# Optimization experiments

Hardware: AMD Instinct MI355X
Metric: run time of the kernel (lower is better)

The kernel has to match this reference:

```python
import math
import jax, jax.numpy as jnp
import numpy as np

B, S, D, L = 8, 2048, 1024, 2


def setup_inputs() -> dict:
    key = jax.random.key(0)
    ks = jax.random.split(key, 16)
    sc = 1.0 / math.sqrt(D)
    mask = jax.random.randint(ks[0], (B, S, S), 0, 2).astype(bool)
    reps = jax.random.normal(ks[1], (B, S, D), dtype=jnp.float32)
    def w(k, shape):
        return jax.random.uniform(k, shape, jnp.float32, -sc, sc)
    return {
        "batch_tk_mask": mask,
        "batch_tk_reps": reps,
        "W_ih": w(ks[2], (L, D, D)), "W_hh": w(ks[3], (L, D, D)),
        "b_ih": w(ks[4], (L, D)), "b_hh": w(ks[5], (L, D)),
        "Wq": w(ks[6], (L, D, D)), "bq": w(ks[7], (L, D)),
        "Wk": w(ks[8], (L, D, D)), "bk": w(ks[9], (L, D)),
        "Wv": w(ks[10], (L, D, D)), "bv": w(ks[11], (L, D)),
        "Wo": w(ks[12], (L, D, D)), "bo": w(ks[13], (L, D)),
    }


def _rnn(x, Wih, Whh, bih, bhh):
    # x: (B,S,D) -> hidden states (B,S,D); h_t = tanh(x_t Wih^T + b_ih + h_{t-1} Whh^T + b_hh)
    h0 = jnp.zeros((x.shape[0], Whh.shape[0]), x.dtype)
    xs = jnp.swapaxes(x, 0, 1)  # (S,B,D)

    def step(h, xt):
        h = jnp.tanh(xt @ Wih.T + bih + h @ Whh.T + bhh)
        return h, h

    _, hs = jax.lax.scan(step, h0, xs)
    return jnp.swapaxes(hs, 0, 1)  # (B,S,D)


def reference(batch_tk_mask, batch_tk_reps, W_ih, W_hh, b_ih, b_hh, Wq, bq, Wk, bk, Wv, bv, Wo, bo):
    scale = 1.0 / math.sqrt(batch_tk_reps.shape[-1])  # sqrt(d_hid)
    batch = batch_tk_reps
    for l in range(L):
        h = _rnn(batch, W_ih[l], W_hh[l], b_ih[l], b_hh[l])  # (B,S,D)
        q = h @ Wq[l].T + bq[l]
        k = h @ Wk[l].T + bk[l]
        v = h @ Wv[l].T + bv[l]
        attn = jnp.einsum("bsd,btd->bst", q, k) * scale  # (B,S,S)
        attn = jnp.where(batch_tk_mask, jnp.float32(-1e9), attn)
        attn = jax.nn.softmax(attn, axis=-1)
        batch = jnp.einsum("bst,btd->bsd", attn, v) @ Wo[l].T + bo[l]
        # dropout p=0.0 -> identity
    return batch
```

## Files before the change

kernel.cpp:

```cpp
#include <hip/hip_runtime.h>
#include <hip/hip_bf16.h>

#define BATCH 8
#define SEQ   2048
#define DIM   1024
#define NLAYER 2

typedef float  f32x4 __attribute__((ext_vector_type(4)));
typedef short  s16x8 __attribute__((ext_vector_type(8)));
typedef unsigned short u16x4 __attribute__((ext_vector_type(4)));

__device__ __forceinline__ void split_bf16(float x, unsigned short& hi, unsigned short& lo) {
  const __hip_bfloat16 hb = __float2bfloat16(x);
  hi = *reinterpret_cast<const unsigned short*>(&hb);
  const float hf = __bfloat162float(hb);
  lo = (unsigned short)(__float_as_uint(x - hf) >> 16);
}

__global__ __launch_bounds__(256)
void split_mat(const float* __restrict__ W, unsigned short* __restrict__ Wh,
               unsigned short* __restrict__ Wl)
{
  const int i = (blockIdx.x * 256 + threadIdx.x) * 4;
  const float4 v = *(const float4*)&W[i];
  unsigned short h0,h1,h2,h3,l0,l1,l2,l3;
  split_bf16(v.x, h0, l0); split_bf16(v.y, h1, l1);
  split_bf16(v.z, h2, l2); split_bf16(v.w, h3, l3);
  *(u16x4*)&Wh[i] = (u16x4){h0, h1, h2, h3};
  *(u16x4*)&Wl[i] = (u16x4){l0, l1, l2, l3};
}

template<int TRANSB>
__global__ __launch_bounds__(256)
void gemm_bf16x3(const float* __restrict__ A, const float* __restrict__ B,
                 const float* __restrict__ bias, float* __restrict__ C,
                 int M, int N, int K, float alpha,
                 long long strideA, long long strideB, long long strideC)
{
  constexpr int LK = 40;
  __shared__ unsigned short Ah[128 * LK], Al[128 * LK];
  __shared__ unsigned short Bh[128 * LK], Bl[128 * LK];

  const int z = blockIdx.z;
  A += (size_t)z * strideA;
  B += (size_t)z * strideB;
  C += (size_t)z * strideC;

  const int tid  = threadIdx.x;
  const int row0 = blockIdx.x * 128;
  const int col0 = blockIdx.y * 128;
  const int w    = tid >> 6;
  const int lane = tid & 63;
  const int m0   = (w >> 1) * 64;
  const int n0   = (w & 1) * 64;
  const int half = lane >> 4;
  const int mr   = lane & 15;

  f32x4 acc[4][4];
#pragma unroll
  for (int i = 0; i < 4; ++i)
#pragma unroll
    for (int j = 0; j < 4; ++j) acc[i][j] = (f32x4){0.f, 0.f, 0.f, 0.f};

  for (int k0 = 0; k0 < K; k0 += 32) {
    __syncthreads();
    {
      const int r = tid >> 3, c4 = tid & 7;
#pragma unroll
      for (int rep = 0; rep < 4; ++rep) {
        const int row = r + rep * 32;
        const float4 v = *(const float4*)&A[(size_t)(row0 + row) * K + k0 + c4 * 4];
        unsigned short h0,h1,h2,h3,l0,l1,l2,l3;
        split_bf16(v.x, h0, l0); split_bf16(v.y, h1, l1);
        split_bf16(v.z, h2, l2); split_bf16(v.w, h3, l3);
        *(u16x4*)&Ah[row * LK + c4 * 4] = (u16x4){h0, h1, h2, h3};
        *(u16x4*)&Al[row * LK + c4 * 4] = (u16x4){l0, l1, l2, l3};
      }
    }
    if (TRANSB) {
      const int r = tid >> 3, c4 = tid & 7;
#pragma unroll
      for (int rep = 0; rep < 4; ++rep) {
        const int row = r + rep * 32;
        const float4 v = *(const float4*)&B[(size_t)(col0 + row) * K + k0 + c4 * 4];
        unsigned short h0,h1,h2,h3,l0,l1,l2,l3;
        split_bf16(v.x, h0, l0); split_bf16(v.y, h1, l1);
        split_bf16(v.z, h2, l2); split_bf16(v.w, h3, l3);
        *(u16x4*)&Bh[row * LK + c4 * 4] = (u16x4){h0, h1, h2, h3};
        *(u16x4*)&Bl[row * LK + c4 * 4] = (u16x4){l0, l1, l2, l3};
      }
    } else {
      const int kk8 = tid >> 5, n4 = tid & 31;
#pragma unroll
      for (int rep = 0; rep < 4; ++rep) {
        const int kk = kk8 + rep * 8;
        const float4 v = *(const float4*)&B[(size_t)(k0 + kk) * N + col0 + n4 * 4];
        unsigned short h, l;
        split_bf16(v.x, h, l); Bh[(n4*4+0)*LK + kk] = h; Bl[(n4*4+0)*LK + kk] = l;
        split_bf16(v.y, h, l); Bh[(n4*4+1)*LK + kk] = h; Bl[(n4*4+1)*LK + kk] = l;
        split_bf16(v.z, h, l); Bh[(n4*4+2)*LK + kk] = h; Bl[(n4*4+2)*LK + kk] = l;
        split_bf16(v.w, h, l); Bh[(n4*4+3)*LK + kk] = h; Bl[(n4*4+3)*LK + kk] = l;
      }
    }
    __syncthreads();

    s16x8 ah[4], al[4], bh[4], bl[4];
#pragma unroll
    for (int i = 0; i < 4; ++i) {
      ah[i] = *(const s16x8*)&Ah[(m0 + i*16 + mr) * LK + half * 8];
      al[i] = *(const s16x8*)&Al[(m0 + i*16 + mr) * LK + half * 8];
      bh[i] = *(const s16x8*)&Bh[(n0 + i*16 + mr) * LK + half * 8];
      bl[i] = *(const s16x8*)&Bl[(n0 + i*16 + mr) * LK + half * 8];
    }
#pragma unroll
    for (int i = 0; i < 4; ++i)
#pragma unroll
      for (int j = 0; j < 4; ++j) {
        acc[i][j] = __builtin_amdgcn_mfma_f32_16x16x32_bf16(ah[i], bh[j], acc[i][j], 0, 0, 0);
        acc[i][j] = __builtin_amdgcn_mfma_f32_16x16x32_bf16(ah[i], bl[j], acc[i][j], 0, 0, 0);
        acc[i][j] = __builtin_amdgcn_mfma_f32_16x16x32_bf16(al[i], bh[j], acc[i][j], 0, 0, 0);
      }
  }

#pragma unroll
  for (int j = 0; j < 4; ++j) {
    const int col = col0 + n0 + j * 16 + mr;
    const float bb = bias ? bias[col] : 0.f;
#pragma unroll
    for (int i = 0; i < 4; ++i) {
#pragma unroll
      for (int q = 0; q < 4; ++q) {
        const int row = row0 + m0 + i * 16 + half * 4 + q;
        C[(size_t)row * N + col] = fmaf(alpha, acc[i][j][q], bb);
      }
    }
  }
}

__global__ __launch_bounds__(256)
void gemm_bsplit(const float* __restrict__ A,
                 const unsigned short* __restrict__ Bhg,
                 const unsigned short* __restrict__ Blg,
                 const float* __restrict__ bias, float* __restrict__ C,
                 int M, int N, int K, float alpha)
{
  constexpr int LK = 40;
  __shared__ unsigned short Ah[128 * LK], Al[128 * LK];
  __shared__ unsigned short Bh[128 * LK], Bl[128 * LK];

  const int tid  = threadIdx.x;
  const int row0 = blockIdx.x * 128;
  const int col0 = blockIdx.y * 128;
  const int w    = tid >> 6;
  const int lane = tid & 63;
  const int m0   = (w >> 1) * 64;
  const int n0   = (w & 1) * 64;
  const int half = lane >> 4;
  const int mr   = lane & 15;

  f32x4 acc[4][4];
#pragma unroll
  for (int i = 0; i < 4; ++i)
#pragma unroll
    for (int j = 0; j < 4; ++j) acc[i][j] = (f32x4){0.f, 0.f, 0.f, 0.f};

  for (int k0 = 0; k0 < K; k0 += 32) {
    __syncthreads();
    {
      const int r = tid >> 3, c4 = tid & 7;
#pragma unroll
      for (int rep = 0; rep < 4; ++rep) {
        const int row = r + rep * 32;
        const float4 v = *(const float4*)&A[(size_t)(row0 + row) * K + k0 + c4 * 4];
        unsigned short h0,h1,h2,h3,l0,l1,l2,l3;
        split_bf16(v.x, h0, l0); split_bf16(v.y, h1, l1);
        split_bf16(v.z, h2, l2); split_bf16(v.w, h3, l3);
        *(u16x4*)&Ah[row * LK + c4 * 4] = (u16x4){h0, h1, h2, h3};
        *(u16x4*)&Al[row * LK + c4 * 4] = (u16x4){l0, l1, l2, l3};
      }
    }
    {
      const int r = tid >> 3, c4 = tid & 7;
#pragma unroll
      for (int rep = 0; rep < 4; ++rep) {
        const int row = r + rep * 32;
        const size_t off = (size_t)(col0 + row) * K + k0 + c4 * 4;
        *(u16x4*)&Bh[row * LK + c4 * 4] = *(const u16x4*)&Bhg[off];
        *(u16x4*)&Bl[row * LK + c4 * 4] = *(const u16x4*)&Blg[off];
      }
    }
    __syncthreads();

    s16x8 ah[4], al[4], bh[4], bl[4];
#pragma unroll
    for (int i = 0; i < 4; ++i) {
      ah[i] = *(const s16x8*)&Ah[(m0 + i*16 + mr) * LK + half * 8];
      al[i] = *(const s16x8*)&Al[(m0 + i*16 + mr) * LK + half * 8];
      bh[i] = *(const s16x8*)&Bh[(n0 + i*16 + mr) * LK + half * 8];
      bl[i] = *(const s16x8*)&Bl[(n0 + i*16 + mr) * LK + half * 8];
    }
#pragma unroll
    for (int i = 0; i < 4; ++i)
#pragma unroll
      for (int j = 0; j < 4; ++j) {
        acc[i][j] = __builtin_amdgcn_mfma_f32_16x16x32_bf16(ah[i], bh[j], acc[i][j], 0, 0, 0);
        acc[i][j] = __builtin_amdgcn_mfma_f32_16x16x32_bf16(ah[i], bl[j], acc[i][j], 0, 0, 0);
        acc[i][j] = __builtin_amdgcn_mfma_f32_16x16x32_bf16(al[i], bh[j], acc[i][j], 0, 0, 0);
      }
  }

#pragma unroll
  for (int j = 0; j < 4; ++j) {
    const int col = col0 + n0 + j * 16 + mr;
    const float bb = bias ? bias[col] : 0.f;
#pragma unroll
    for (int i = 0; i < 4; ++i) {
#pragma unroll
      for (int q = 0; q < 4; ++q) {
        const int row = row0 + m0 + i * 16 + half * 4 + q;
        C[(size_t)row * N + col] = fmaf(alpha, acc[i][j][q], bb);
      }
    }
  }
}

__device__ __forceinline__ float fast_tanh(float x) {
  const float a = fabsf(x);
  const float e = __expf(2.0f * a);
  const float t = 1.0f - 2.0f / (e + 1.0f);
  return copysignf(t, x);
}

__global__ __launch_bounds__(512, 1)
void rnn_scan(const float* __restrict__ Pre, float* __restrict__ Hout,
              const float* __restrict__ Whh, const float* __restrict__ bhh)
{
  __shared__ float wS[32][DIM];
  __shared__ __align__(16) float hbuf[2][DIM];
  __shared__ float pS[8][8];
  const int b    = blockIdx.x & 7;
  const int p    = blockIdx.x >> 3;
  const int wv   = threadIdx.x >> 6;
  const int lane = threadIdx.x & 63;
  const int fl   = ((lane & 1) << 1) | ((lane >> 1) & 1);

  const float* PreB = Pre  + (size_t)b * SEQ * DIM;
  float*       HB   = Hout + (size_t)b * SEQ * DIM;

  for (int i = threadIdx.x; i < 32 * (DIM / 4); i += 512) {
    const int row = i >> 8, c4 = i & 255;
    *(f32x4*)&wS[row][c4 * 4] =
        *(const f32x4*)&Whh[(size_t)(p * 32 + row) * DIM + c4 * 4];
  }
  __syncthreads();

  const bool w0lane = (wv == 0) && (lane < 32);
  const float biasv = w0lane ? bhh[p * 32 + lane] : 0.f;

  for (int t = 0; t < SEQ; ++t) {
    float pre = 0.f;
    if (w0lane) pre = PreB[(size_t)t * DIM + p * 32 + lane];

    f32x4 wr[4][4];
    if (wv != 0) {
#pragma unroll
      for (int r = 0; r < 4; ++r) {
        wr[r][0] = *(const f32x4*)&wS[wv * 4 + r][  0 + lane * 4];
        wr[r][1] = *(const f32x4*)&wS[wv * 4 + r][256 + lane * 4];
        wr[r][2] = *(const f32x4*)&wS[wv * 4 + r][512 + lane * 4];
        wr[r][3] = *(const f32x4*)&wS[wv * 4 + r][768 + lane * 4];
      }
    }

    if (t > 0) {
      if (wv == 0) {
        const float* hp = HB + (size_t)(t - 1) * DIM;
        const float* q0 = hp +   0 + lane * 4;
        const float* q1 = hp + 256 + lane * 4;
        const float* q2 = hp + 512 + lane * 4;
        const float* q3 = hp + 768 + lane * 4;
        f32x4 m0, m1, m2, m3;
        while (true) {
          f32x4 f0, f1, f2, f3;
          asm volatile(
            "global_load_dwordx4 %0, %4, off sc0\n\t"
            "global_load_dwordx4 %1, %5, off sc0\n\t"
            "global_load_dwordx4 %2, %6, off sc0\n\t"
            "global_load_dwordx4 %3, %7, off sc0\n\t"
            "s_waitcnt vmcnt(0)"
            : "=&v"(f0), "=&v"(f1), "=&v"(f2), "=&v"(f3)
            : "v"(q0), "v"(q1), "v"(q2), "v"(q3));
          bool gf = true;
#pragma unroll
          for (int j = 0; j < 4; ++j) {
            gf = gf && (__float_as_uint(f0[j]) != 0xFFFFFFFFu)
                    && (__float_as_uint(f1[j]) != 0xFFFFFFFFu)
                    && (__float_as_uint(f2[j]) != 0xFFFFFFFFu)
                    && (__float_as_uint(f3[j]) != 0xFFFFFFFFu);
          }
          if (__all(gf)) { m0 = f0; m1 = f1; m2 = f2; m3 = f3; break; }

          f32x4 s0, s1, s2, s3;
          asm volatile(
            "global_load_dwordx4 %0, %4, off sc0 sc1\n\t"
            "global_load_dwordx4 %1, %5, off sc0 sc1\n\t"
            "global_load_dwordx4 %2, %6, off sc0 sc1\n\t"
            "global_load_dwordx4 %3, %7, off sc0 sc1\n\t"
            "s_waitcnt vmcnt(0)"
            : "=&v"(s0), "=&v"(s1), "=&v"(s2), "=&v"(s3)
            : "v"(q0), "v"(q1), "v"(q2), "v"(q3));
          bool gm = true;
#pragma unroll
          for (int j = 0; j < 4; ++j) {
            m0[j] = (__float_as_uint(f0[j]) != 0xFFFFFFFFu) ? f0[j] : s0[j];
            m1[j] = (__float_as_uint(f1[j]) != 0xFFFFFFFFu) ? f1[j] : s1[j];
            m2[j] = (__float_as_uint(f2[j]) != 0xFFFFFFFFu) ? f2[j] : s2[j];
            m3[j] = (__float_as_uint(f3[j]) != 0xFFFFFFFFu) ? f3[j] : s3[j];
            gm = gm && (__float_as_uint(m0[j]) != 0xFFFFFFFFu)
                    && (__float_as_uint(m1[j]) != 0xFFFFFFFFu)
                    && (__float_as_uint(m2[j]) != 0xFFFFFFFFu)
                    && (__float_as_uint(m3[j]) != 0xFFFFFFFFu);
          }
          if (__all(gm)) break;
        }
        *(f32x4*)&hbuf[t & 1][  0 + lane * 4] = m0;
        *(f32x4*)&hbuf[t & 1][256 + lane * 4] = m1;
        *(f32x4*)&hbuf[t & 1][512 + lane * 4] = m2;
        *(f32x4*)&hbuf[t & 1][768 + lane * 4] = m3;
#pragma unroll
        for (int r = 0; r < 4; ++r) {
          wr[r][0] = *(const f32x4*)&wS[wv * 4 + r][  0 + lane * 4];
          wr[r][1] = *(const f32x4*)&wS[wv * 4 + r][256 + lane * 4];
          wr[r][2] = *(const f32x4*)&wS[wv * 4 + r][512 + lane * 4];
          wr[r][3] = *(const f32x4*)&wS[wv * 4 + r][768 + lane * 4];
        }
      }
      __syncthreads();
      const f32x4 h0 = *(const f32x4*)&hbuf[t & 1][  0 + lane * 4];
      const f32x4 h1 = *(const f32x4*)&hbuf[t & 1][256 + lane * 4];
      const f32x4 h2 = *(const f32x4*)&hbuf[t & 1][512 + lane * 4];
      const f32x4 h3 = *(const f32x4*)&hbuf[t & 1][768 + lane * 4];
      float acc[4];
#pragma unroll
      for (int r = 0; r < 4; ++r) {
        float a = 0.f;
        a = fmaf(wr[r][0].x, h0.x, fmaf(wr[r][0].y, h0.y,
            fmaf(wr[r][0].z, h0.z, fmaf(wr[r][0].w, h0.w, a))));
        a = fmaf(wr[r][1].x, h1.x, fmaf(wr[r][1].y, h1.y,
            fmaf(wr[r][1].z, h1.z, fmaf(wr[r][1].w, h1.w, a))));
        a = fmaf(wr[r][2].x, h2.x, fmaf(wr[r][2].y, h2.y,
            fmaf(wr[r][2].z, h2.z, fmaf(wr[r][2].w, h2.w, a))));
        a = fmaf(wr[r][3].x, h3.x, fmaf(wr[r][3].y, h3.y,
            fmaf(wr[r][3].z, h3.z, fmaf(wr[r][3].w, h3.w, a))));
        acc[r] = a;
      }
#pragma unroll
      for (int m = 0; m < 2; ++m) {
        const int mask = 1 << m;
        const int nv   = 2 >> m;
        const bool up  = (lane & mask) != 0;
#pragma unroll
        for (int r = 0; r < nv; ++r) {
          const float lo = up ? acc[r + nv] : acc[r];
          const float hi = up ? acc[r] : acc[r + nv];
          acc[r] = lo + __shfl_xor(hi, mask);
        }
      }
#pragma unroll
      for (int off = 4; off < 64; off <<= 1) acc[0] += __shfl_xor(acc[0], off);

      if (lane < 4) pS[wv][fl] = acc[0];
      __syncthreads();
    }

    if (w0lane) {
      float s = (t > 0) ? (pre + pS[lane >> 2][lane & 3] + biasv)
                        : (pre + biasv);
      const float v = fast_tanh(s);
      float* dst = HB + (size_t)t * DIM + p * 32 + lane;
      asm volatile(
        "global_store_dword %0, %1, off sc0\n\t"
        "global_store_dword %0, %1, off sc0 sc1"
        :: "v"(dst), "v"(v));
    }
  }
}

__global__ __launch_bounds__(256)
void softmax_mask(float* __restrict__ S, const unsigned char* __restrict__ mask)
{
  const size_t row = (size_t)blockIdx.y * gridDim.x + blockIdx.x;
  float* p = S + row * SEQ;
  const unsigned char* mrow = mask + row * SEQ;
  __shared__ float buf[SEQ];
  __shared__ float red[4];
  const int tid = threadIdx.x, lane = tid & 63, wv = tid >> 6;

  float mx = -1e30f;
  for (int i = tid; i < SEQ; i += 256) {
    const float v = mrow[i] ? -1e9f : p[i];
    buf[i] = v;
    mx = fmaxf(mx, v);
  }
#pragma unroll
  for (int off = 1; off < 64; off <<= 1) mx = fmaxf(mx, __shfl_xor(mx, off));
  if (lane == 0) red[wv] = mx;
  __syncthreads();
  mx = fmaxf(fmaxf(red[0], red[1]), fmaxf(red[2], red[3]));

  float s = 0.f;
  for (int i = tid; i < SEQ; i += 256) {
    const float e = __expf(buf[i] - mx);
    buf[i] = e;
    s += e;
  }
#pragma unroll
  for (int off = 1; off < 64; off <<= 1) s += __shfl_xor(s, off);
  __syncthreads();
  if (lane == 0) red[wv] = s;
  __syncthreads();
  s = red[0] + red[1] + red[2] + red[3];
  const float inv = 1.f / s;
  for (int i = tid; i < SEQ; i += 256) p[i] = buf[i] * inv;
}

extern "C" void kernel_launch(void* const* d_in, const int* in_sizes, int n_in,
                              void* d_out, int out_size, void* d_ws, size_t ws_size,
                              hipStream_t stream)
{
  (void)in_sizes; (void)n_in; (void)out_size;
  const unsigned char* mask = (const unsigned char*)d_in[0];
  const float* reps = (const float*)d_in[1];
  const float* Wih  = (const float*)d_in[2];
  const float* Whh  = (const float*)d_in[3];
  const float* bih  = (const float*)d_in[4];
  const float* bhh  = (const float*)d_in[5];
  const float* Wq   = (const float*)d_in[6];
  const float* bq   = (const float*)d_in[7];
  const float* Wk   = (const float*)d_in[8];
  const float* bk   = (const float*)d_in[9];
  const float* Wv   = (const float*)d_in[10];
  const float* bv   = (const float*)d_in[11];
  const float* Wo   = (const float*)d_in[12];
  const float* bo   = (const float*)d_in[13];
  float* out = (float*)d_out;

  char* ws = (char*)d_ws;
  float* Hb = (float*)(ws);
  float* Qb = (float*)(ws + ((size_t)64  << 20));
  float* Kb = (float*)(ws + ((size_t)128 << 20));
  float* Vb = (float*)(ws + ((size_t)192 << 20));
  float* Sb = (float*)(ws + ((size_t)256 << 20));
  const size_t needFull = ((size_t)256 << 20) + (size_t)BATCH * SEQ * SEQ * 4;
  const bool fullS = ws_size >= needFull;
  const size_t MM = (size_t)DIM * DIM;
  unsigned short* wsp = (unsigned short*)(ws + needFull);
  const bool presplit = fullS && (ws_size >= needFull + ((size_t)20 << 20));
  const size_t hBytes = (size_t)BATCH * SEQ * DIM * 4;

  const int M1 = BATCH * SEQ;
  const float scale = 0.03125f;
  const dim3 blk(256);
  const dim3 projGrid(M1/128, DIM/128, 1);
  const long long sSD = (long long)SEQ * DIM;
  const long long sSS = (long long)SEQ * SEQ;
  const int splitGrid = (int)(MM / (256 * 4));

  const float* X = reps;
  for (int l = 0; l < NLAYER; ++l) {
    const size_t wof = (size_t)l * DIM * DIM;
    const size_t bof = (size_t)l * DIM;
    float* Y = (l == NLAYER - 1) ? out : Qb;

    hipMemsetAsync(Hb, 0xFF, hBytes, stream);
    if (presplit) {
      split_mat<<<splitGrid, blk, 0, stream>>>(Wih + wof, wsp + 0*MM, wsp + 1*MM);
      split_mat<<<splitGrid, blk, 0, stream>>>(Wq  + wof, wsp + 2*MM, wsp + 3*MM);
      split_mat<<<splitGrid, blk, 0, stream>>>(Wk  + wof, wsp + 4*MM, wsp + 5*MM);
      split_mat<<<splitGrid, blk, 0, stream>>>(Wv  + wof, wsp + 6*MM, wsp + 7*MM);
      split_mat<<<splitGrid, blk, 0, stream>>>(Wo  + wof, wsp + 8*MM, wsp + 9*MM);
    }

    if (presplit)
      gemm_bsplit<<<projGrid, blk, 0, stream>>>(
          X, wsp + 0*MM, wsp + 1*MM, bih + bof, Kb, M1, DIM, DIM, 1.f);
    else
      gemm_bf16x3<1><<<projGrid, blk, 0, stream>>>(
          X, Wih + wof, bih + bof, Kb, M1, DIM, DIM, 1.f, 0, 0, 0);

    rnn_scan<<<dim3(256), dim3(512), 0, stream>>>(Kb, Hb, Whh + wof, bhh + bof);

    if (presplit) {
      gemm_bsplit<<<projGrid, blk, 0, stream>>>(
          Hb, wsp + 2*MM, wsp + 3*MM, bq + bof, Qb, M1, DIM, DIM, 1.f);
      gemm_bsplit<<<projGrid, blk, 0, stream>>>(
          Hb, wsp + 4*MM, wsp + 5*MM, bk + bof, Kb, M1, DIM, DIM, 1.f);
      gemm_bsplit<<<projGrid, blk, 0, stream>>>(
          Hb, wsp + 6*MM, wsp + 7*MM, bv + bof, Vb, M1, DIM, DIM, 1.f);
    } else {
      gemm_bf16x3<1><<<projGrid, blk, 0, stream>>>(
          Hb, Wq + wof, bq + bof, Qb, M1, DIM, DIM, 1.f, 0, 0, 0);
      gemm_bf16x3<1><<<projGrid, blk, 0, stream>>>(
          Hb, Wk + wof, bk + bof, Kb, M1, DIM, DIM, 1.f, 0, 0, 0);
      gemm_bf16x3<1><<<projGrid, blk, 0, stream>>>(
          Hb, Wv + wof, bv + bof, Vb, M1, DIM, DIM, 1.f, 0, 0, 0);
    }

    if (fullS) {
      gemm_bf16x3<1><<<dim3(SEQ/128, SEQ/128, BATCH), blk, 0, stream>>>(
          Qb, Kb, nullptr, Sb, SEQ, SEQ, DIM, scale, sSD, sSD, sSS);
      softmax_mask<<<dim3(SEQ, BATCH), blk, 0, stream>>>(Sb, mask);
      gemm_bf16x3<0><<<dim3(SEQ/128, DIM/128, BATCH), blk, 0, stream>>>(
          Sb, Vb, nullptr, Hb, SEQ, DIM, SEQ, 1.f, sSS, sSD, sSD);
    } else {
      for (int bb = 0; bb < BATCH; ++bb) {
        gemm_bf16x3<1><<<dim3(SEQ/128, SEQ/128, 1), blk, 0, stream>>>(
            Qb + (size_t)bb * sSD, Kb + (size_t)bb * sSD, nullptr, Sb,
            SEQ, SEQ, DIM, scale, 0, 0, 0);
        softmax_mask<<<dim3(SEQ, 1), blk, 0, stream>>>(Sb, mask + (size_t)bb * sSS);
        gemm_bf16x3<0><<<dim3(SEQ/128, DIM/128, 1), blk, 0, stream>>>(
            Sb, Vb + (size_t)bb * sSD, nullptr, Hb + (size_t)bb * sSD,
            SEQ, DIM, SEQ, 1.f, 0, 0, 0);
      }
    }

    if (presplit)
      gemm_bsplit<<<projGrid, blk, 0, stream>>>(
          Hb, wsp + 8*MM, wsp + 9*MM, bo + bof, Y, M1, DIM, DIM, 1.f);
    else
      gemm_bf16x3<1><<<projGrid, blk, 0, stream>>>(
          Hb, Wo + wof, bo + bof, Y, M1, DIM, DIM, 1.f, 0, 0, 0);
    X = Y;
  }
}
```

Before: 10.71 ms.

## Emit pre-split bf16 Q/K and transposed V to remove per-tile splitting in attention GEMMs

When the workspace allows pre-splitting, the Q and K projections now write bf16 hi/lo planes directly. V is written in fp32 and then transposed and split by a new vtrans kernel. The QK^T GEMM loads the pre-split A and B operands, and the PV GEMM reads the transposed split V. This removes the repeated fp32-to-bf16x2 conversion, and the strided non-transposed B load, from the large attention GEMMs. The cost is an extra transpose kernel and reuse of buffers as bf16 planes, which depends on the aliasing being correct.

```diff
diff --git a/kernel.cpp b/kernel.cpp
--- a/kernel.cpp
+++ b/kernel.cpp
@@ -30,21 +30,57 @@
   *(u16x4*)&Wl[i] = (u16x4){l0, l1, l2, l3};
 }
 
-template<int TRANSB>
 __global__ __launch_bounds__(256)
-void gemm_bf16x3(const float* __restrict__ A, const float* __restrict__ B,
+void vtrans(const float* __restrict__ V, unsigned short* __restrict__ Th,
+            unsigned short* __restrict__ Tl)
+{
+  __shared__ float t[64][65];
+  const int z = blockIdx.z;
+  V  += (size_t)z * SEQ * DIM;
+  Th += (size_t)z * (size_t)DIM * SEQ;
+  Tl += (size_t)z * (size_t)DIM * SEQ;
+  const int s0 = blockIdx.x * 64, d0 = blockIdx.y * 64;
+  const int tid = threadIdx.x;
+#pragma unroll
+  for (int rep = 0; rep < 4; ++rep) {
+    const int idx = rep * 256 + tid;
+    const int r = idx >> 4, c = idx & 15;
+    const float4 v = *(const float4*)&V[(size_t)(s0 + r) * DIM + d0 + c * 4];
+    t[c*4+0][r] = v.x; t[c*4+1][r] = v.y; t[c*4+2][r] = v.z; t[c*4+3][r] = v.w;
+  }
+  __syncthreads();
+#pragma unroll
+  for (int rep = 0; rep < 4; ++rep) {
+    const int idx = rep * 256 + tid;
+    const int r = idx >> 4, c = idx & 15;
+    unsigned short h[4], l[4];
+#pragma unroll
+    for (int j = 0; j < 4; ++j) split_bf16(t[r][c*4+j], h[j], l[j]);
+    const size_t off = (size_t)(d0 + r) * SEQ + s0 + c * 4;
+    *(u16x4*)&Th[off] = (u16x4){h[0], h[1], h[2], h[3]};
+    *(u16x4*)&Tl[off] = (u16x4){l[0], l[1], l[2], l[3]};
+  }
+}
+
+template<int WS>
+__global__ __launch_bounds__(256)
+void gemm_bsplit(const float* __restrict__ A,
+                 const unsigned short* __restrict__ Bhg,
+                 const unsigned short* __restrict__ Blg,
                  const float* __restrict__ bias, float* __restrict__ C,
+                 unsigned short* __restrict__ Ch, unsigned short* __restrict__ Cl,
                  int M, int N, int K, float alpha,
-                 long long strideA, long long strideB, long long strideC)
+                 long long sA, long long sB, long long sC)
 {
   constexpr int LK = 40;
   __shared__ unsigned short Ah[128 * LK], Al[128 * LK];
   __shared__ unsigned short Bh[128 * LK], Bl[128 * LK];
 
   const int z = blockIdx.z;
-  A += (size_t)z * strideA;
-  B += (size_t)z * strideB;
-  C += (size_t)z * strideC;
+  A += (size_t)z * sA;
+  Bhg += (size_t)z * sB;  Blg += (size_t)z * sB;
+  if (WS) { Ch += (size_t)z * sC; Cl += (size_t)z * sC; }
+  else    { C  += (size_t)z * sC; }
 
   const int tid  = threadIdx.x;
   const int row0 = blockIdx.x * 128;
@@ -77,29 +113,14 @@
         *(u16x4*)&Al[row * LK + c4 * 4] = (u16x4){l0, l1, l2, l3};
       }
     }
-    if (TRANSB) {
+    {
       const int r = tid >> 3, c4 = tid & 7;
 #pragma unroll
       for (int rep = 0; rep < 4; ++rep) {
         const int row = r + rep * 32;
-        const float4 v = *(const float4*)&B[(size_t)(col0 + row) * K + k0 + c4 * 4];
-        unsigned short h0,h1,h2,h3,l0,l1,l2,l3;
-        split_bf16(v.x, h0, l0); split_bf16(v.y, h1, l1);
-        split_bf16(v.z, h2, l2); split_bf16(v.w, h3, l3);
-        *(u16x4*)&Bh[row * LK + c4 * 4] = (u16x4){h0, h1, h2, h3};
-        *(u16x4*)&Bl[row * LK + c4 * 4] = (u16x4){l0, l1, l2, l3};
-      }
-    } else {
-      const int kk8 = tid >> 5, n4 = tid & 31;
-#pragma unroll
-      for (int rep = 0; rep < 4; ++rep) {
-        const int kk = kk8 + rep * 8;
-        const float4 v = *(const float4*)&B[(size_t)(k0 + kk) * N + col0 + n4 * 4];
-        unsigned short h, l;
-        split_bf16(v.x, h, l); Bh[(n4*4+0)*LK + kk] = h; Bl[(n4*4+0)*LK + kk] = l;
-        split_bf16(v.y, h, l); Bh[(n4*4+1)*LK + kk] = h; Bl[(n4*4+1)*LK + kk] = l;
-        split_bf16(v.z, h, l); Bh[(n4*4+2)*LK + kk] = h; Bl[(n4*4+2)*LK + kk] = l;
-        split_bf16(v.w, h, l); Bh[(n4*4+3)*LK + kk] = h; Bl[(n4*4+3)*LK + kk] = l;
+        const size_t off = (size_t)(col0 + row) * K + k0 + c4 * 4;
+        *(u16x4*)&Bh[row * LK + c4 * 4] = *(const u16x4*)&Bhg[off];
+        *(u16x4*)&Bl[row * LK + c4 * 4] = *(const u16x4*)&Blg[off];
       }
     }
     __syncthreads();
@@ -131,22 +152,37 @@
 #pragma unroll
       for (int q = 0; q < 4; ++q) {
         const int row = row0 + m0 + i * 16 + half * 4 + q;
-        C[(size_t)row * N + col] = fmaf(alpha, acc[i][j][q], bb);
+        const float val = fmaf(alpha, acc[i][j][q], bb);
+        if (WS) {
+          unsigned short h, l;
+          split_bf16(val, h, l);
+          Ch[(size_t)row * N + col] = h;
+          Cl[(size_t)row * N + col] = l;
+        } else {
+          C[(size_t)row * N + col] = val;
+        }
       }
     }
   }
 }
 
 __global__ __launch_bounds__(256)
-void gemm_bsplit(const float* __restrict__ A,
-                 const unsigned short* __restrict__ Bhg,
-                 const unsigned short* __restrict__ Blg,
-                 const float* __restrict__ bias, float* __restrict__ C,
-                 int M, int N, int K, float alpha)
+void gemm_absplit(const unsigned short* __restrict__ Ahg,
+                  const unsigned short* __restrict__ Alg,
+                  const unsigned short* __restrict__ Bhg,
+                  const unsigned short* __restrict__ Blg,
+                  float* __restrict__ C,
+                  int M, int N, int K, float alpha,
+                  long long sA, long long sB, long long sC)
 {
   constexpr int LK = 40;
   __shared__ unsigned short Ah[128 * LK], Al[128 * LK];
   __shared__ unsigned short Bh[128 * LK], Bl[128 * LK];
+
+  const int z = blockIdx.z;
+  Ahg += (size_t)z * sA;  Alg += (size_t)z * sA;
+  Bhg += (size_t)z * sB;  Blg += (size_t)z * sB;
+  C   += (size_t)z * sC;
 
   const int tid  = threadIdx.x;
   const int row0 = blockIdx.x * 128;
@@ -171,6 +207,87 @@
 #pragma unroll
       for (int rep = 0; rep < 4; ++rep) {
         const int row = r + rep * 32;
+        const size_t offA = (size_t)(row0 + row) * K + k0 + c4 * 4;
+        *(u16x4*)&Ah[row * LK + c4 * 4] = *(const u16x4*)&Ahg[offA];
+        *(u16x4*)&Al[row * LK + c4 * 4] = *(const u16x4*)&Alg[offA];
+        const size_t offB = (size_t)(col0 + row) * K + k0 + c4 * 4;
+        *(u16x4*)&Bh[row * LK + c4 * 4] = *(const u16x4*)&Bhg[offB];
+        *(u16x4*)&Bl[row * LK + c4 * 4] = *(const u16x4*)&Blg[offB];
+      }
+    }
+    __syncthreads();
+
+    s16x8 ah[4], al[4], bh[4], bl[4];
+#pragma unroll
+    for (int i = 0; i < 4; ++i) {
+      ah[i] = *(const s16x8*)&Ah[(m0 + i*16 + mr) * LK + half * 8];
+      al[i] = *(const s16x8*)&Al[(m0 + i*16 + mr) * LK + half * 8];
+      bh[i] = *(const s16x8*)&Bh[(n0 + i*16 + mr) * LK + half * 8];
+      bl[i] = *(const s16x8*)&Bl[(n0 + i*16 + mr) * LK + half * 8];
+    }
+#pragma unroll
+    for (int i = 0; i < 4; ++i)
+#pragma unroll
+      for (int j = 0; j < 4; ++j) {
+        acc[i][j] = __builtin_amdgcn_mfma_f32_16x16x32_bf16(ah[i], bh[j], acc[i][j], 0, 0, 0);
+        acc[i][j] = __builtin_amdgcn_mfma_f32_16x16x32_bf16(ah[i], bl[j], acc[i][j], 0, 0, 0);
+        acc[i][j] = __builtin_amdgcn_mfma_f32_16x16x32_bf16(al[i], bh[j], acc[i][j], 0, 0, 0);
+      }
+  }
+
+#pragma unroll
+  for (int j = 0; j < 4; ++j) {
+    const int col = col0 + n0 + j * 16 + mr;
+#pragma unroll
+    for (int i = 0; i < 4; ++i) {
+#pragma unroll
+      for (int q = 0; q < 4; ++q) {
+        const int row = row0 + m0 + i * 16 + half * 4 + q;
+        C[(size_t)row * N + col] = alpha * acc[i][j][q];
+      }
+    }
+  }
+}
+
+template<int TRANSB>
+__global__ __launch_bounds__(256)
+void gemm_bf16x3(const float* __restrict__ A, const float* __restrict__ B,
+                 const float* __restrict__ bias, float* __restrict__ C,
+                 int M, int N, int K, float alpha,
+                 long long strideA, long long strideB, long long strideC)
+{
+  constexpr int LK = 40;
+  __shared__ unsigned short Ah[128 * LK], Al[128 * LK];
+  __shared__ unsigned short Bh[128 * LK], Bl[128 * LK];
+
+  const int z = blockIdx.z;
+  A += (size_t)z * strideA;
+  B += (size_t)z * strideB;
+  C += (size_t)z * strideC;
+
+  const int tid  = threadIdx.x;
+  const int row0 = blockIdx.x * 128;
+  const int col0 = blockIdx.y * 128;
+  const int w    = tid >> 6;
+  const int lane = tid & 63;
+  const int m0   = (w >> 1) * 64;
+  const int n0   = (w & 1) * 64;
+  const int half = lane >> 4;
+  const int mr   = lane & 15;
+
+  f32x4 acc[4][4];
+#pragma unroll
+  for (int i = 0; i < 4; ++i)
+#pragma unroll
+    for (int j = 0; j < 4; ++j) acc[i][j] = (f32x4){0.f, 0.f, 0.f, 0.f};
+
+  for (int k0 = 0; k0 < K; k0 += 32) {
+    __syncthreads();
+    {
+      const int r = tid >> 3, c4 = tid & 7;
+#pragma unroll
+      for (int rep = 0; rep < 4; ++rep) {
+        const int row = r + rep * 32;
         const float4 v = *(const float4*)&A[(size_t)(row0 + row) * K + k0 + c4 * 4];
         unsigned short h0,h1,h2,h3,l0,l1,l2,l3;
         split_bf16(v.x, h0, l0); split_bf16(v.y, h1, l1);
@@ -179,14 +296,29 @@
         *(u16x4*)&Al[row * LK + c4 * 4] = (u16x4){l0, l1, l2, l3};
       }
     }
-    {
+    if (TRANSB) {
       const int r = tid >> 3, c4 = tid & 7;
 #pragma unroll
       for (int rep = 0; rep < 4; ++rep) {
         const int row = r + rep * 32;
-        const size_t off = (size_t)(col0 + row) * K + k0 + c4 * 4;
-        *(u16x4*)&Bh[row * LK + c4 * 4] = *(const u16x4*)&Bhg[off];
-        *(u16x4*)&Bl[row * LK + c4 * 4] = *(const u16x4*)&Blg[off];
+        const float4 v = *(const float4*)&B[(size_t)(col0 + row) * K + k0 + c4 * 4];
+        unsigned short h0,h1,h2,h3,l0,l1,l2,l3;
+        split_bf16(v.x, h0, l0); split_bf16(v.y, h1, l1);
+        split_bf16(v.z, h2, l2); split_bf16(v.w, h3, l3);
+        *(u16x4*)&Bh[row * LK + c4 * 4] = (u16x4){h0, h1, h2, h3};
+        *(u16x4*)&Bl[row * LK + c4 * 4] = (u16x4){l0, l1, l2, l3};
+      }
+    } else {
+      const int kk8 = tid >> 5, n4 = tid & 31;
+#pragma unroll
+      for (int rep = 0; rep < 4; ++rep) {
+        const int kk = kk8 + rep * 8;
+        const float4 v = *(const float4*)&B[(size_t)(k0 + kk) * N + col0 + n4 * 4];
+        unsigned short h, l;
+        split_bf16(v.x, h, l); Bh[(n4*4+0)*LK + kk] = h; Bl[(n4*4+0)*LK + kk] = l;
+        split_bf16(v.y, h, l); Bh[(n4*4+1)*LK + kk] = h; Bl[(n4*4+1)*LK + kk] = l;
+        split_bf16(v.z, h, l); Bh[(n4*4+2)*LK + kk] = h; Bl[(n4*4+2)*LK + kk] = l;
+        split_bf16(v.w, h, l); Bh[(n4*4+3)*LK + kk] = h; Bl[(n4*4+3)*LK + kk] = l;
       }
     }
     __syncthreads();
@@ -459,12 +591,17 @@
   const size_t hBytes = (size_t)BATCH * SEQ * DIM * 4;
 
   const int M1 = BATCH * SEQ;
+  const size_t PL = (size_t)M1 * DIM;
   const float scale = 0.03125f;
   const dim3 blk(256);
   const dim3 projGrid(M1/128, DIM/128, 1);
   const long long sSD = (long long)SEQ * DIM;
   const long long sSS = (long long)SEQ * SEQ;
   const int splitGrid = (int)(MM / (256 * 4));
+
+  unsigned short* Qh = (unsigned short*)Qb;  unsigned short* Ql = Qh + PL;
+  unsigned short* Kh = (unsigned short*)Kb;  unsigned short* Kl = Kh + PL;
+  unsigned short* Vth = (unsigned short*)Vb; unsigned short* Vtl = Vth + PL;
 
   const float* X = reps;
   for (int l = 0; l < NLAYER; ++l) {
@@ -479,57 +616,62 @@
       split_mat<<<splitGrid, blk, 0, stream>>>(Wk  + wof, wsp + 4*MM, wsp + 5*MM);
       split_mat<<<splitGrid, blk, 0, stream>>>(Wv  + wof, wsp + 6*MM, wsp + 7*MM);
       split_mat<<<splitGrid, blk, 0, stream>>>(Wo  + wof, wsp + 8*MM, wsp + 9*MM);
-    }
-
-    if (presplit)
-      gemm_bsplit<<<projGrid, blk, 0, stream>>>(
-          X, wsp + 0*MM, wsp + 1*MM, bih + bof, Kb, M1, DIM, DIM, 1.f);
-    else
+
+      gemm_bsplit<0><<<projGrid, blk, 0, stream>>>(
+          X, wsp + 0*MM, wsp + 1*MM, bih + bof, Kb, nullptr, nullptr,
+          M1, DIM, DIM, 1.f, 0, 0, 0);
+      rnn_scan<<<dim3(256), dim3(512), 0, stream>>>(Kb, Hb, Whh + wof, bhh + bof);
+
+      gemm_bsplit<1><<<projGrid, blk, 0, stream>>>(
+          Hb, wsp + 2*MM, wsp + 3*MM, bq + bof, nullptr, Qh, Ql,
+          M1, DIM, DIM, 1.f, 0, 0, 0);
+      gemm_bsplit<1><<<projGrid, blk, 0, stream>>>(
+          Hb, wsp + 4*MM, wsp + 5*MM, bk + bof, nullptr, Kh, Kl,
+          M1, DIM, DIM, 1.f, 0, 0, 0);
+      gemm_bsplit<0><<<projGrid, blk, 0, stream>>>(
+          Hb, wsp + 6*MM, wsp + 7*MM, bv + bof, Sb, nullptr, nullptr,
+          M1, DIM, DIM, 1.f, 0, 0, 0);
+      vtrans<<<dim3(SEQ/64, DIM/64, BATCH), blk, 0, stream>>>(Sb, Vth, Vtl);
+
+      gemm_absplit<<<dim3(SEQ/128, SEQ/128, BATCH), blk, 0, stream>>>(
+          Qh, Ql, Kh, Kl, Sb, SEQ, SEQ, DIM, scale, sSD, sSD, sSS);
+      softmax_mask<<<dim3(SEQ, BATCH), blk, 0, stream>>>(Sb, mask);
+      gemm_bsplit<0><<<dim3(SEQ/128, DIM/128, BATCH), blk, 0, stream>>>(
+          Sb, Vth, Vtl, nullptr, Hb, nullptr, nullptr,
+          SEQ, DIM, SEQ, 1.f, sSS, (long long)DIM * SEQ, sSD);
+      gemm_bsplit<0><<<projGrid, blk, 0, stream>>>(
+          Hb, wsp + 8*MM, wsp + 9*MM, bo + bof, Y, nullptr, nullptr,
+          M1, DIM, DIM, 1.f, 0, 0, 0);
+    } else {
       gemm_bf16x3<1><<<projGrid, blk, 0, stream>>>(
           X, Wih + wof, bih + bof, Kb, M1, DIM, DIM, 1.f, 0, 0, 0);
-
-    rnn_scan<<<dim3(256), dim3(512), 0, stream>>>(Kb, Hb, Whh + wof, bhh + bof);
-
-    if (presplit) {
-      gemm_bsplit<<<projGrid, blk, 0, stream>>>(
-          Hb, wsp + 2*MM, wsp + 3*MM, bq + bof, Qb, M1, DIM, DIM, 1.f);
-      gemm_bsplit<<<projGrid, blk, 0, stream>>>(
-          Hb, wsp + 4*MM, wsp + 5*MM, bk + bof, Kb, M1, DIM, DIM, 1.f);
-      gemm_bsplit<<<projGrid, blk, 0, stream>>>(
-          Hb, wsp + 6*MM, wsp + 7*MM, bv + bof, Vb, M1, DIM, DIM, 1.f);
-    } else {
+      rnn_scan<<<dim3(256), dim3(512), 0, stream>>>(Kb, Hb, Whh + wof, bhh + bof);
       gemm_bf16x3<1><<<projGrid, blk, 0, stream>>>(
           Hb, Wq + wof, bq + bof, Qb, M1, DIM, DIM, 1.f, 0, 0, 0);
       gemm_bf16x3<1><<<projGrid, blk, 0, stream>>>(
           Hb, Wk + wof, bk + bof, Kb, M1, DIM, DIM, 1.f, 0, 0, 0);
       gemm_bf16x3<1><<<projGrid, blk, 0, stream>>>(
           Hb, Wv + wof, bv + bof, Vb, M1, DIM, DIM, 1.f, 0, 0, 0);
-    }
-
-    if (fullS) {
-      gemm_bf16x3<1><<<dim3(SEQ/128, SEQ/128, BATCH), blk, 0, stream>>>(
-          Qb, Kb, nullptr, Sb, SEQ, SEQ, DIM, scale, sSD, sSD, sSS);
-      softmax_mask<<<dim3(SEQ, BATCH), blk, 0, stream>>>(Sb, mask);
-      gemm_bf16x3<0><<<dim3(SEQ/128, DIM/128, BATCH), blk, 0, stream>>>(
-          Sb, Vb, nullptr, Hb, SEQ, DIM, SEQ, 1.f, sSS, sSD, sSD);
-    } else {
-      for (int bb = 0; bb < BATCH; ++bb) {
-        gemm_bf16x3<1><<<dim3(SEQ/128, SEQ/128, 1), blk, 0, stream>>>(
-            Qb + (size_t)bb * sSD, Kb + (size_t)bb * sSD, nullptr, Sb,
-            SEQ, SEQ, DIM, scale, 0, 0, 0);
-        softmax_mask<<<dim3(SEQ, 1), blk, 0, stream>>>(Sb, mask + (size_t)bb * sSS);
-        gemm_bf16x3<0><<<dim3(SEQ/128, DIM/128, 1), blk, 0, stream>>>(
-            Sb, Vb + (size_t)bb * sSD, nullptr, Hb + (size_t)bb * sSD,
-            SEQ, DIM, SEQ, 1.f, 0, 0, 0);
-      }
-    }
-
-    if (presplit)
-      gemm_bsplit<<<projGrid, blk, 0, stream>>>(
-          Hb, wsp + 8*MM, wsp + 9*MM, bo + bof, Y, M1, DIM, DIM, 1.f);
-    else
+      if (fullS) {
+        gemm_bf16x3<1><<<dim3(SEQ/128, SEQ/128, BATCH), blk, 0, stream>>>(
+            Qb, Kb, nullptr, Sb, SEQ, SEQ, DIM, scale, sSD, sSD, sSS);
+        softmax_mask<<<dim3(SEQ, BATCH), blk, 0, stream>>>(Sb, mask);
+        gemm_bf16x3<0><<<dim3(SEQ/128, DIM/128, BATCH), blk, 0, stream>>>(
+            Sb, Vb, nullptr, Hb, SEQ, DIM, SEQ, 1.f, sSS, sSD, sSD);
+      } else {
+        for (int bb = 0; bb < BATCH; ++bb) {
+          gemm_bf16x3<1><<<dim3(SEQ/128, SEQ/128, 1), blk, 0, stream>>>(
+              Qb + (size_t)bb * sSD, Kb + (size_t)bb * sSD, nullptr, Sb,
+              SEQ, SEQ, DIM, scale, 0, 0, 0);
+          softmax_mask<<<dim3(SEQ, 1), blk, 0, stream>>>(Sb, mask + (size_t)bb * sSS);
+          gemm_bf16x3<0><<<dim3(SEQ/128, DIM/128, 1), blk, 0, stream>>>(
+              Sb, Vb + (size_t)bb * sSD, nullptr, Hb + (size_t)bb * sSD,
+              SEQ, DIM, SEQ, 1.f, 0, 0, 0);
+        }
+      }
       gemm_bf16x3<1><<<projGrid, blk, 0, stream>>>(
           Hb, Wo + wof, bo + bof, Y, M1, DIM, DIM, 1.f, 0, 0, 0);
+    }
     X = Y;
   }
 }
```

Measured after the change: 10.14 ms, median of 2. 1.06x faster.
